# Performance work log

Hardware: AMD Instinct MI355X
Metric: run time of the kernel (lower is better)

## Reference

```python
import jax, jax.numpy as jnp
import numpy as np

B, S, DIM = 2, 2048, 4096
NH, NKV, HD = 32, 8, 128
N_REP = NH // NKV


def apply_rope(x, cos, sin):
    # x: [B, S, H, HD]; cos/sin: [S, HD//2]
    xp = x.reshape(*x.shape[:-1], HD // 2, 2)
    xr, xi = xp[..., 0], xp[..., 1]
    c = cos[None, :, None, :]
    s = sin[None, :, None, :]
    orr = xr * c - xi * s
    oi = xr * s + xi * c
    return jnp.stack([orr, oi], axis=-1).reshape(x.shape)


def setup_inputs() -> dict:
    key = jax.random.key(0)
    ks = jax.random.split(key, 8)
    scale = 1.0 / np.sqrt(DIM)
    return {
        "x": jax.random.normal(ks[0], (B, S, DIM), jnp.float32),
        "wq": jax.random.normal(ks[1], (DIM, NH * HD), jnp.float32) * scale,
        "wk": jax.random.normal(ks[2], (DIM, NKV * HD), jnp.float32) * scale,
        "wv": jax.random.normal(ks[3], (DIM, NKV * HD), jnp.float32) * scale,
        "wo": jax.random.normal(ks[4], (NH * HD, DIM), jnp.float32) * scale,
        "freqs_cos": jnp.cos(jnp.arange(S, dtype=jnp.float32)[:, None]
                             * (1.0 / (10000.0 ** (jnp.arange(0, HD, 2, dtype=jnp.float32) / HD)))[None, :]),
        "freqs_sin": jnp.sin(jnp.arange(S, dtype=jnp.float32)[:, None]
                             * (1.0 / (10000.0 ** (jnp.arange(0, HD, 2, dtype=jnp.float32) / HD)))[None, :]),
        "cache_k": jnp.zeros((B, S, NKV, HD), jnp.float32),
        "cache_v": jnp.zeros((B, S, NKV, HD), jnp.float32),
        "start_pos": 0,
    }


def reference(x, wq, wk, wv, wo, freqs_cos, freqs_sin, cache_k, cache_v, start_pos):
    b, s, _ = x.shape
    xq = (x @ wq).reshape(b, s, NH, HD)
    xk = (x @ wk).reshape(b, s, NKV, HD)
    xv = (x @ wv).reshape(b, s, NKV, HD)
    xq = apply_rope(xq, freqs_cos, freqs_sin)
    xk = apply_rope(xk, freqs_cos, freqs_sin)
    # KV-cache append (start_pos is a static Python int)
    cache_k = jax.lax.dynamic_update_slice(cache_k, xk, (0, start_pos, 0, 0))
    cache_v = jax.lax.dynamic_update_slice(cache_v, xv, (0, start_pos, 0, 0))
    t = start_pos + s
    keys = cache_k[:, :t]    # [B, T, NKV, HD]
    values = cache_v[:, :t]
    # GQA attention without materializing repeated KV
    q = xq.transpose(0, 2, 1, 3).reshape(b, NKV, N_REP, s, HD)  # [B, K, R, S, HD]
    k = keys.transpose(0, 2, 1, 3)    # [B, K, T, HD]
    v = values.transpose(0, 2, 1, 3)  # [B, K, T, HD]
    inv_sqrt = 1.0 / np.sqrt(HD)
    scores = jnp.einsum('bkrsd,bktd->bkrst', q, k * inv_sqrt)  # keys scaled, as in original
    probs = jax.nn.softmax(scores.astype(jnp.float32), axis=-1).astype(q.dtype)
    out = jnp.einsum('bkrst,bktd->bkrsd', probs, v)  # [B, K, R, S, HD]
    out = out.reshape(b, NH, s, HD).transpose(0, 2, 1, 3).reshape(b, s, NH * HD)
    return out @ wo
```

## Files before the change

kernel.cpp:

```cpp
#include <hip/hip_runtime.h>
#include <cstdint>
#include <cstddef>

#define B_    2
#define S_    2048
#define DIM_  4096
#define NH_   32
#define NKV_  8
#define HD_   128

typedef short bf16x8 __attribute__((ext_vector_type(8)));
typedef float f32x4  __attribute__((ext_vector_type(4)));

__device__ __forceinline__ short f2bf(float x) {
  unsigned u = __builtin_bit_cast(unsigned, x);
  u += 0x7fffu + ((u >> 16) & 1u);
  return (short)(u >> 16);
}
__device__ __forceinline__ float bf2f(short s) {
  unsigned u = ((unsigned)(unsigned short)s) << 16;
  return __builtin_bit_cast(float, u);
}

#define GLDS(gp, lp) __builtin_amdgcn_global_load_lds( \
    (const __attribute__((address_space(1))) void*)(gp), \
    (__attribute__((address_space(3))) void*)(lp), 16, 0, 0)

__global__ void cast_x(const float* __restrict__ in, short* __restrict__ out) {
  int i = (blockIdx.x * 256 + threadIdx.x) * 4;
  const float4 v = *(const float4*)(in + i);
  short4 o;
  o.x = f2bf(v.x); o.y = f2bf(v.y); o.z = f2bf(v.z); o.w = f2bf(v.w);
  *(short4*)(out + i) = o;
}

__global__ void tcast(const float* __restrict__ W, short* __restrict__ Wt, int K, int N) {
  __shared__ float t[32][33];
  int tid = threadIdx.x;
  int r = tid >> 3, c4 = (tid & 7) << 2;
  int n0 = blockIdx.x << 5, k0 = blockIdx.y << 5;
  const float4 v = *(const float4*)(W + (size_t)(k0 + r) * N + n0 + c4);
  t[r][c4] = v.x; t[r][c4 + 1] = v.y; t[r][c4 + 2] = v.z; t[r][c4 + 3] = v.w;
  __syncthreads();
  short4 o;
  o.x = f2bf(t[c4][r]); o.y = f2bf(t[c4 + 1][r]);
  o.z = f2bf(t[c4 + 2][r]); o.w = f2bf(t[c4 + 3][r]);
  *(short4*)(Wt + (size_t)(n0 + r) * K + k0 + c4) = o;
}

template <int OUT_BF16>
__global__ __launch_bounds__(256) void gemm_bt(const short* __restrict__ A,
                                               const short* __restrict__ Bt,
                                               float* __restrict__ Cf,
                                               short* __restrict__ Cb,
                                               int M, int N, int K) {
  __shared__ __align__(16) short As[128 * 32];
  __shared__ __align__(16) short Bs[128 * 32];
  const int tid = threadIdx.x;
  const int wave = tid >> 6, lane = tid & 63;
  const int quad = lane >> 4, l16 = lane & 15;
  const int bm = blockIdx.y << 7, bn = blockIdx.x << 7;
  const int wm = (wave >> 1) << 6, wn = (wave & 1) << 6;

  f32x4 acc[4][4];
  for (int i = 0; i < 4; ++i)
    for (int j = 0; j < 4; ++j)
      for (int r = 0; r < 4; ++r) acc[i][j][r] = 0.f;

  const int sw = quad ^ ((l16 >> 1) & 3);

  for (int k0 = 0; k0 < K; k0 += 32) {
    __syncthreads();
#pragma unroll
    for (int rr = 0; rr < 2; ++rr) {
      const int idb = rr * 256 + wave * 64;
      const int id = idb + lane;
      const int ar = id >> 2;
      const int ac = (id & 3) ^ ((ar >> 1) & 3);
      GLDS(A  + (size_t)(bm + ar) * K + k0 + ac * 8, As + idb * 8);
      GLDS(Bt + (size_t)(bn + ar) * K + k0 + ac * 8, Bs + idb * 8);
    }
    __syncthreads();

    bf16x8 af[4], bfr[4];
#pragma unroll
    for (int i = 0; i < 4; ++i)
      af[i] = *(const bf16x8*)(As + ((wm + i * 16 + l16) * 4 + sw) * 8);
#pragma unroll
    for (int i = 0; i < 4; ++i)
      bfr[i] = *(const bf16x8*)(Bs + ((wn + i * 16 + l16) * 4 + sw) * 8);
#pragma unroll
    for (int mi = 0; mi < 4; ++mi)
#pragma unroll
      for (int ni = 0; ni < 4; ++ni)
        acc[mi][ni] = __builtin_amdgcn_mfma_f32_16x16x32_bf16(af[mi], bfr[ni],
                                                              acc[mi][ni], 0, 0, 0);
  }
#pragma unroll
  for (int mi = 0; mi < 4; ++mi)
#pragma unroll
    for (int ni = 0; ni < 4; ++ni)
#pragma unroll
      for (int r = 0; r < 4; ++r) {
        int row = bm + wm + mi * 16 + quad * 4 + r;
        int col = bn + wn + ni * 16 + l16;
        size_t off = (size_t)row * N + col;
        if (OUT_BF16) Cb[off] = f2bf(acc[mi][ni][r]);
        else          Cf[off] = acc[mi][ni][r];
      }
}

#define STAGE_HALF(G, row0, k0, Sdst) do { \
  _Pragma("unroll") \
  for (int rr_ = 0; rr_ < 2; ++rr_) { \
    const int idb_ = rr_ * 512 + wave * 64; \
    const int id_ = idb_ + lane; \
    const int r_ = id_ >> 3, c_ = id_ & 7; \
    GLDS((G) + (size_t)((row0) + r_) * 4096 + (k0) + ((c_ ^ (r_ & 7)) * 8), \
         (Sdst) + idb_ * 8); \
  } \
} while (0)

#define LOADA8(dst, ABp, QM) do { \
  _Pragma("unroll") \
  for (int mi_ = 0; mi_ < 4; ++mi_) { \
    _Pragma("unroll") \
    for (int ks_ = 0; ks_ < 2; ++ks_) \
      dst[mi_][ks_] = *(const bf16x8*)((ABp) + ((QM) * 128 + wr * 64 + mi_ * 16 + l16) * 64 \
                                            + (((ks_ * 4 + quad) ^ l7s) * 8)); \
  } \
} while (0)

#define LOADB4(dst, BBp, QN) do { \
  _Pragma("unroll") \
  for (int ni_ = 0; ni_ < 2; ++ni_) { \
    _Pragma("unroll") \
    for (int ks_ = 0; ks_ < 2; ++ks_) \
      dst[ni_][ks_] = *(const bf16x8*)((BBp) + ((QN) * 128 + wc * 32 + ni_ * 16 + l16) * 64 \
                                            + (((ks_ * 4 + quad) ^ l7s) * 8)); \
  } \
} while (0)

#define MFMA16(QM, QN, afv, bqv) do { \
  __builtin_amdgcn_s_setprio(1); \
  _Pragma("unroll") \
  for (int mi_ = 0; mi_ < 4; ++mi_) { \
    _Pragma("unroll") \
    for (int ni_ = 0; ni_ < 2; ++ni_) { \
      acc[QM][QN][mi_][ni_] = __builtin_amdgcn_mfma_f32_16x16x32_bf16( \
          afv[mi_][0], bqv[ni_][0], acc[QM][QN][mi_][ni_], 0, 0, 0); \
      acc[QM][QN][mi_][ni_] = __builtin_amdgcn_mfma_f32_16x16x32_bf16( \
          afv[mi_][1], bqv[ni_][1], acc[QM][QN][mi_][ni_], 0, 0, 0); \
    } \
  } \
  __builtin_amdgcn_s_setprio(0); \
} while (0)

#define SYNC_IN  __builtin_amdgcn_s_barrier(); \
                 asm volatile("s_waitcnt lgkmcnt(0)" ::: "memory"); \
                 __builtin_amdgcn_sched_barrier(0);
#define SYNC_OUT __builtin_amdgcn_sched_barrier(0); \
                 __builtin_amdgcn_s_barrier();

#define TILE4(AB, BB, S0, S1, S2, S3, TAIL) do { \
  bf16x8 af[4][2], bq0[2][2], bq1[2][2]; \
  LOADA8(af, AB, 0); LOADB4(bq0, BB, 0); S0 SYNC_IN MFMA16(0, 0, af, bq0); SYNC_OUT \
  LOADB4(bq1, BB, 1);                    S1 SYNC_IN MFMA16(0, 1, af, bq1); SYNC_OUT \
  LOADA8(af, AB, 1);                     S2 SYNC_IN MFMA16(1, 1, af, bq1); SYNC_OUT \
                                         S3 SYNC_IN MFMA16(1, 0, af, bq0); TAIL SYNC_OUT \
} while (0)

template <int OUT_BF16>
__global__ __launch_bounds__(512, 2) void gemm256(const short* __restrict__ A,
                                                  const short* __restrict__ Bt,
                                                  float* __restrict__ Cf,
                                                  short* __restrict__ Cb,
                                                  int N) {
  __shared__ __align__(16) short As0[256 * 64];
  __shared__ __align__(16) short Bs0[256 * 64];
  __shared__ __align__(16) short As1[256 * 64];
  __shared__ __align__(16) short Bs1[256 * 64];
  const int tid = threadIdx.x;
  const int wave = tid >> 6, lane = tid & 63;
  const int quad = lane >> 4, l16 = lane & 15, l7s = l16 & 7;
  const int wr = wave >> 2, wc = wave & 3;
  const int bm = blockIdx.y << 8, bn = blockIdx.x << 8;

  f32x4 acc[2][2][4][2];
#pragma unroll
  for (int a = 0; a < 2; ++a)
#pragma unroll
    for (int b = 0; b < 2; ++b)
#pragma unroll
      for (int c = 0; c < 4; ++c)
#pragma unroll
        for (int d = 0; d < 2; ++d)
#pragma unroll
          for (int r = 0; r < 4; ++r) acc[a][b][c][d][r] = 0.f;

  STAGE_HALF(A,  bm,       0,  As0);
  STAGE_HALF(Bt, bn,       0,  Bs0);
  STAGE_HALF(A,  bm + 128, 0,  As0 + 8192);
  STAGE_HALF(Bt, bn + 128, 0,  Bs0 + 8192);
  STAGE_HALF(A,  bm,       64, As1);
  STAGE_HALF(Bt, bn + 128, 64, Bs1 + 8192);
  asm volatile("s_waitcnt vmcnt(4)" ::: "memory");
  __builtin_amdgcn_s_barrier();

#pragma clang loop unroll(disable)
  for (int tt = 0; tt < 31; ++tt) {
    const int k1 = (2 * tt + 1) << 6, k2 = (2 * tt + 2) << 6, k3 = (2 * tt + 3) << 6;
    TILE4(As0, Bs0,
          STAGE_HALF(A,  bm + 128, k1, As1 + 8192);,
          STAGE_HALF(Bt, bn,       k1, Bs1);,
          STAGE_HALF(A,  bm,       k2, As0);,
          STAGE_HALF(Bt, bn + 128, k2, Bs0 + 8192);,
          asm volatile("s_waitcnt vmcnt(4)" ::: "memory"););
    TILE4(As1, Bs1,
          STAGE_HALF(A,  bm + 128, k2, As0 + 8192);,
          STAGE_HALF(Bt, bn,       k2, Bs0);,
          STAGE_HALF(A,  bm,       k3, As1);,
          STAGE_HALF(Bt, bn + 128, k3, Bs1 + 8192);,
          asm volatile("s_waitcnt vmcnt(4)" ::: "memory"););
  }
  TILE4(As0, Bs0,
        STAGE_HALF(A,  bm + 128, 4032, As1 + 8192);,
        STAGE_HALF(Bt, bn,       4032, Bs1);,
        ;, ;,
        asm volatile("s_waitcnt vmcnt(0)" ::: "memory"););
  TILE4(As1, Bs1, ;, ;, ;, ;, ;);

#pragma unroll
  for (int qm = 0; qm < 2; ++qm)
#pragma unroll
    for (int qn = 0; qn < 2; ++qn)
#pragma unroll
      for (int mi = 0; mi < 4; ++mi)
#pragma unroll
        for (int ni = 0; ni < 2; ++ni)
#pragma unroll
          for (int r = 0; r < 4; ++r) {
            int row = bm + qm * 128 + wr * 64 + mi * 16 + quad * 4 + r;
            int col = bn + qn * 128 + wc * 32 + ni * 16 + l16;
            size_t off = (size_t)row * N + col;
            if (OUT_BF16) Cb[off] = f2bf(acc[qm][qn][mi][ni][r]);
            else          Cf[off] = acc[qm][qn][mi][ni][r];
          }
}

#define QSCALE 0.12751745444105413f
__global__ void rope_pack_q(const short* __restrict__ xq, const float* __restrict__ fc,
                            const float* __restrict__ fs, short* __restrict__ qp) {
  int i = blockIdx.x * 256 + threadIdx.x;
  int d = i & 63; int t = i >> 6;
  int h = t & (NH_ - 1); t >>= 5;
  int s = t & (S_ - 1);  int b = t >> 11;
  size_t src = ((size_t)((b * S_ + s) * NH_ + h)) * HD_ + 2 * d;
  unsigned rv = *(const unsigned*)(xq + src);
  float xr = bf2f((short)(rv & 0xffff)), xi = bf2f((short)(rv >> 16));
  float c = fc[s * 64 + d], sn = fs[s * 64 + d];
  float orr = (xr * c - xi * sn) * QSCALE, oi = (xr * sn + xi * c) * QSCALE;
  size_t dst = ((size_t)((b * NH_ + h) * S_ + s)) * HD_ + 2 * d;
  unsigned pv = (unsigned)(unsigned short)f2bf(orr) |
                ((unsigned)(unsigned short)f2bf(oi) << 16);
  *(unsigned*)(qp + dst) = pv;
}

__global__ void rope_pack_k(const short* __restrict__ xk, const float* __restrict__ fc,
                            const float* __restrict__ fs, short* __restrict__ kp) {
  int i = blockIdx.x * 256 + threadIdx.x;
  int d = i & 63; int t = i >> 6;
  int kh = t & (NKV_ - 1); t >>= 3;
  int s = t & (S_ - 1); int b = t >> 11;
  size_t src = ((size_t)((b * S_ + s) * NKV_ + kh)) * HD_ + 2 * d;
  unsigned rv = *(const unsigned*)(xk + src);
  float xr = bf2f((short)(rv & 0xffff)), xi = bf2f((short)(rv >> 16));
  float c = fc[s * 64 + d], sn = fs[s * 64 + d];
  float orr = xr * c - xi * sn, oi = xr * sn + xi * c;
  size_t dst = ((size_t)((b * NKV_ + kh) * S_ + s)) * HD_ + 2 * d;
  unsigned pv = (unsigned)(unsigned short)f2bf(orr) |
                ((unsigned)(unsigned short)f2bf(oi) << 16);
  *(unsigned*)(kp + dst) = pv;
}

__global__ void pack_v(const short* __restrict__ xv, short* __restrict__ vt) {
  int i = blockIdx.x * 256 + threadIdx.x;
  int p = i & (S_ - 1); int t = i >> 11;
  int hd = t & (HD_ - 1); t >>= 7;
  int kh = t & (NKV_ - 1); int b = t >> 3;
  vt[i] = xv[((size_t)(b * S_ + p) * NKV_ + kh) * HD_ + hd];
}

__global__ __launch_bounds__(512) void attn(const short* __restrict__ Qp,
                                            const short* __restrict__ Kp,
                                            const short* __restrict__ Vt,
                                            short* __restrict__ AO) {
  __shared__ __align__(16) short Ks[64 * 128];
  __shared__ __align__(16) short Vs[128 * 64];
  __shared__ __align__(16) short Ps[8][16 * 64];
  const int tid = threadIdx.x, wave = tid >> 6, lane = tid & 63;
  const int quad = lane >> 4, l16 = lane & 15;
  const int qt = blockIdx.x, h = blockIdx.y, b = blockIdx.z;
  const int kh = h >> 2;
  const short* Qh = Qp + ((size_t)(b * NH_ + h) * S_) * HD_;
  const short* Kh = Kp + ((size_t)(b * NKV_ + kh) * S_) * HD_;
  const short* Vh = Vt + ((size_t)(b * NKV_ + kh) * HD_) * S_;

  const int qrow = qt * 128 + wave * 16 + l16;
  bf16x8 qf[4];
#pragma unroll
  for (int ks = 0; ks < 4; ++ks)
    qf[ks] = *(const bf16x8*)(Qh + (size_t)qrow * HD_ + ks * 32 + quad * 8);

  f32x4 o[8];
  for (int i = 0; i < 8; ++i)
    for (int r = 0; r < 4; ++r) o[i][r] = 0.f;
  float lsum = 0.f;
  const int l7 = l16 & 7;
  short* Pw = &Ps[wave][0];

#pragma clang loop unroll(disable)
  for (int t0 = 0; t0 < S_; t0 += 64) {
    __syncthreads();
#pragma unroll
    for (int rr = 0; rr < 2; ++rr) {
      int idb = rr * 512 + wave * 64;
      int id = idb + lane;
      int kr = id >> 4, kc = (id & 15) ^ (kr & 7);
      GLDS(Kh + (size_t)(t0 + kr) * HD_ + kc * 8, Ks + idb * 8);
      int vr = id >> 3, vc = (id & 7) ^ (vr & 7);
      GLDS(Vh + (size_t)vr * S_ + t0 + vc * 8, Vs + idb * 8);
    }
    __syncthreads();

#pragma unroll
    for (int kb = 0; kb < 4; ++kb) {
      f32x4 a;
      for (int r = 0; r < 4; ++r) a[r] = 0.f;
      __builtin_amdgcn_s_setprio(1);
#pragma unroll
      for (int ks = 0; ks < 4; ++ks) {
        bf16x8 kf = *(const bf16x8*)(Ks + ((kb * 16 + l16) * 16 +
                                           ((ks * 4 + quad) ^ l7)) * 8);
        a = __builtin_amdgcn_mfma_f32_16x16x32_bf16(kf, qf[ks], a, 0, 0, 0);
      }
      __builtin_amdgcn_s_setprio(0);
      float p0 = __builtin_amdgcn_exp2f(a[0]);
      float p1 = __builtin_amdgcn_exp2f(a[1]);
      float p2 = __builtin_amdgcn_exp2f(a[2]);
      float p3 = __builtin_amdgcn_exp2f(a[3]);
      lsum += (p0 + p1) + (p2 + p3);
      unsigned w0 = (unsigned)(unsigned short)f2bf(p0) |
                    ((unsigned)(unsigned short)f2bf(p1) << 16);
      unsigned w1 = (unsigned)(unsigned short)f2bf(p2) |
                    ((unsigned)(unsigned short)f2bf(p3) << 16);
      int c16 = (kb * 2 + (quad >> 1)) ^ l7;
      uint2 wv; wv.x = w0; wv.y = w1;
      *(uint2*)(Pw + l16 * 64 + c16 * 8 + (quad & 1) * 4) = wv;
    }

    __builtin_amdgcn_s_setprio(1);
#pragma unroll
    for (int ks = 0; ks < 2; ++ks) {
      bf16x8 pf = *(const bf16x8*)(Pw + (l16 * 8 + ((ks * 4 + quad) ^ l7)) * 8);
#pragma unroll
      for (int ob = 0; ob < 8; ++ob) {
        bf16x8 vf = *(const bf16x8*)(Vs + ((ob * 16 + l16) * 8 +
                                           ((ks * 4 + quad) ^ l7)) * 8);
        o[ob] = __builtin_amdgcn_mfma_f32_16x16x32_bf16(vf, pf, o[ob], 0, 0, 0);
      }
    }
    __builtin_amdgcn_s_setprio(0);
  }

  lsum += __shfl_xor(lsum, 16, 64);
  lsum += __shfl_xor(lsum, 32, 64);
  float linv = __builtin_amdgcn_rcpf(lsum);
#pragma unroll
  for (int ob = 0; ob < 8; ++ob) {
    short4 s4;
    s4.x = f2bf(o[ob][0] * linv);
    s4.y = f2bf(o[ob][1] * linv);
    s4.z = f2bf(o[ob][2] * linv);
    s4.w = f2bf(o[ob][3] * linv);
    *(short4*)(AO + ((size_t)b * S_ + qrow) * (NH_ * HD_) + h * HD_ +
               ob * 16 + quad * 4) = s4;
  }
}

extern "C" void kernel_launch(void* const* d_in, const int* in_sizes, int n_in,
                              void* d_out, int out_size, void* d_ws, size_t ws_size,
                              hipStream_t stream) {
  (void)in_sizes; (void)n_in; (void)out_size; (void)ws_size;
  const float* x  = (const float*)d_in[0];
  const float* wq = (const float*)d_in[1];
  const float* wk = (const float*)d_in[2];
  const float* wv = (const float*)d_in[3];
  const float* wo = (const float*)d_in[4];
  const float* fc = (const float*)d_in[5];
  const float* fs = (const float*)d_in[6];
  float* out = (float*)d_out;

  char* ws = (char*)d_ws;
  short* xb  = (short*)(ws + 0);
  short* wqt = (short*)(ws + 33554432);
  short* wkt = (short*)(ws + 67108864);
  short* wvt = (short*)(ws + 75497472);
  short* wot = (short*)(ws + 83886080);
  short* xq  = (short*)(ws + 117440512);
  short* xk  = (short*)(ws + 150994944);
  short* xv  = (short*)(ws + 159383552);
  short* kp  = (short*)(ws + 167772160);
  short* vt  = (short*)(ws + 176160768);
  short* qp = xb;
  short* ao = xq;

  cast_x<<<16384, 256, 0, stream>>>(x, xb);
  tcast<<<dim3(128, 128), 256, 0, stream>>>(wq, wqt, 4096, 4096);
  tcast<<<dim3(32, 128),  256, 0, stream>>>(wk, wkt, 4096, 1024);
  tcast<<<dim3(32, 128),  256, 0, stream>>>(wv, wvt, 4096, 1024);
  tcast<<<dim3(128, 128), 256, 0, stream>>>(wo, wot, 4096, 4096);

  gemm256<1><<<dim3(16, 16), 512, 0, stream>>>(xb, wqt, nullptr, xq, 4096);
  gemm_bt<1><<<dim3(8, 32),  256, 0, stream>>>(xb, wkt, nullptr, xk, 4096, 1024, 4096);
  gemm_bt<1><<<dim3(8, 32),  256, 0, stream>>>(xb, wvt, nullptr, xv, 4096, 1024, 4096);

  rope_pack_q<<<32768, 256, 0, stream>>>(xq, fc, fs, qp);
  rope_pack_k<<<8192,  256, 0, stream>>>(xk, fc, fs, kp);
  pack_v<<<16384, 256, 0, stream>>>(xv, vt);

  attn<<<dim3(16, 32, 2), 512, 0, stream>>>(qp, kp, vt, ao);

  gemm256<0><<<dim3(16, 16), 512, 0, stream>>>(ao, wot, out, nullptr, 4096);
}
```

Before: 881.2 us.

## Software-pipeline LDS fragment loads into MFMA phases and deepen global prefetch

Restructures the GEMM main loop so that LDS fragment reads for the next quadrant (and the next tile's first A fragment) are issued inside the same barrier phase as the current MFMAs, rather than before each sync. Global stages for a tile are grouped two per phase and the prologue prefetches a full extra k-tile, with the waitcnt adjusted to match. The aim is to hide LDS read latency behind matrix math and reduce the number of exposed stall points. In exchange, register pressure rises because fragments stay live across phases, and the waitcnt and barrier ordering must stay correct for the double-buffered LDS to avoid races.

```diff
diff --git a/kernel.cpp b/kernel.cpp
--- a/kernel.cpp
+++ b/kernel.cpp
@@ -141,7 +141,7 @@
   } \
 } while (0)
 
-#define MFMA16(QM, QN, afv, bqv) do { \
+#define MFMA16S(QM, QN, afv, bqv) do { \
   __builtin_amdgcn_s_setprio(1); \
   _Pragma("unroll") \
   for (int mi_ = 0; mi_ < 4; ++mi_) { \
@@ -162,12 +162,26 @@
 #define SYNC_OUT __builtin_amdgcn_sched_barrier(0); \
                  __builtin_amdgcn_s_barrier();
 
-#define TILE4(AB, BB, S0, S1, S2, S3, TAIL) do { \
-  bf16x8 af[4][2], bq0[2][2], bq1[2][2]; \
-  LOADA8(af, AB, 0); LOADB4(bq0, BB, 0); S0 SYNC_IN MFMA16(0, 0, af, bq0); SYNC_OUT \
-  LOADB4(bq1, BB, 1);                    S1 SYNC_IN MFMA16(0, 1, af, bq1); SYNC_OUT \
-  LOADA8(af, AB, 1);                     S2 SYNC_IN MFMA16(1, 1, af, bq1); SYNC_OUT \
-                                         S3 SYNC_IN MFMA16(1, 0, af, bq0); TAIL SYNC_OUT \
+#define TILE(Ac, Bc, An, SY, SX, VM, PN) do { \
+  LOADB4(bq0, Bc, 0); \
+  SYNC_IN                                    \
+  MFMA16S(0, 0, af, bq0); \
+  LOADB4(bq1, Bc, 1); \
+  SYNC_OUT \
+  SYNC_IN                                    \
+  MFMA16S(0, 1, af, bq1); \
+  LOADA8(af, Ac, 1); \
+  SYNC_OUT \
+  SYNC_IN                                    \
+  SY \
+  MFMA16S(1, 1, af, bq1); \
+  VM \
+  SYNC_OUT \
+  SYNC_IN                                    \
+  SX \
+  MFMA16S(1, 0, af, bq0); \
+  PN \
+  SYNC_OUT \
 } while (0)
 
 template <int OUT_BF16>
@@ -198,37 +212,39 @@
 #pragma unroll
           for (int r = 0; r < 4; ++r) acc[a][b][c][d][r] = 0.f;
 
+  bf16x8 af[4][2], bq0[2][2], bq1[2][2];
+
   STAGE_HALF(A,  bm,       0,  As0);
   STAGE_HALF(Bt, bn,       0,  Bs0);
   STAGE_HALF(A,  bm + 128, 0,  As0 + 8192);
   STAGE_HALF(Bt, bn + 128, 0,  Bs0 + 8192);
   STAGE_HALF(A,  bm,       64, As1);
   STAGE_HALF(Bt, bn + 128, 64, Bs1 + 8192);
-  asm volatile("s_waitcnt vmcnt(4)" ::: "memory");
+  STAGE_HALF(A,  bm + 128, 64, As1 + 8192);
+  STAGE_HALF(Bt, bn,       64, Bs1);
+  asm volatile("s_waitcnt vmcnt(8)" ::: "memory");
   __builtin_amdgcn_s_barrier();
+  LOADA8(af, As0, 0);
 
 #pragma clang loop unroll(disable)
   for (int tt = 0; tt < 31; ++tt) {
-    const int k1 = (2 * tt + 1) << 6, k2 = (2 * tt + 2) << 6, k3 = (2 * tt + 3) << 6;
-    TILE4(As0, Bs0,
-          STAGE_HALF(A,  bm + 128, k1, As1 + 8192);,
-          STAGE_HALF(Bt, bn,       k1, Bs1);,
-          STAGE_HALF(A,  bm,       k2, As0);,
-          STAGE_HALF(Bt, bn + 128, k2, Bs0 + 8192);,
-          asm volatile("s_waitcnt vmcnt(4)" ::: "memory"););
-    TILE4(As1, Bs1,
-          STAGE_HALF(A,  bm + 128, k2, As0 + 8192);,
-          STAGE_HALF(Bt, bn,       k2, Bs0);,
-          STAGE_HALF(A,  bm,       k3, As1);,
-          STAGE_HALF(Bt, bn + 128, k3, Bs1 + 8192);,
-          asm volatile("s_waitcnt vmcnt(4)" ::: "memory"););
+    const int kE = (2 * tt + 2) << 6;
+    const int kO = (2 * tt + 3) << 6;
+    TILE(As0, Bs0, As1,
+         STAGE_HALF(A, bm, kE, As0); STAGE_HALF(Bt, bn + 128, kE, Bs0 + 8192);,
+         STAGE_HALF(A, bm + 128, kE, As0 + 8192); STAGE_HALF(Bt, bn, kE, Bs0);,
+         asm volatile("s_waitcnt vmcnt(4)" ::: "memory");,
+         LOADA8(af, As1, 0););
+    TILE(As1, Bs1, As0,
+         STAGE_HALF(A, bm, kO, As1); STAGE_HALF(Bt, bn + 128, kO, Bs1 + 8192);,
+         STAGE_HALF(A, bm + 128, kO, As1 + 8192); STAGE_HALF(Bt, bn, kO, Bs1);,
+         asm volatile("s_waitcnt vmcnt(4)" ::: "memory");,
+         LOADA8(af, As0, 0););
   }
-  TILE4(As0, Bs0,
-        STAGE_HALF(A,  bm + 128, 4032, As1 + 8192);,
-        STAGE_HALF(Bt, bn,       4032, Bs1);,
-        ;, ;,
-        asm volatile("s_waitcnt vmcnt(0)" ::: "memory"););
-  TILE4(As1, Bs1, ;, ;, ;, ;, ;);
+  TILE(As0, Bs0, As1, ;, ;,
+       asm volatile("s_waitcnt vmcnt(0)" ::: "memory");,
+       LOADA8(af, As1, 0););
+  TILE(As1, Bs1, As0, ;, ;, ;, ;);
 
 #pragma unroll
   for (int qm = 0; qm < 2; ++qm)
```

Measured after the change: 850.9 us. 3.4% less time.
